# Optimization experiments

Measured on AMD Instinct MI355X. Metric: run time of the kernel, lower is better.

The kernel has to match this reference:

```python
import jax, jax.numpy as jnp
import numpy as np

NEG = -1e30  # finite stand-in for -inf (grad-safe)
GAMMA = 2.0
ALPHA = 1.0


def setup_inputs() -> dict:
    key = jax.random.key(0)
    k1, k2, k3 = jax.random.split(key, 3)
    N, T, C, S = 128, 64, 6625, 25
    logits = jax.random.normal(k1, (N, T, C), dtype=jnp.float32)
    # labels exclude blank (=0)
    targets = jax.random.randint(k2, (N, S), 1, C)
    target_length = jax.random.randint(k3, (N,), 1, S + 1)
    return {"logits": logits, "targets": targets, "target_length": target_length}


def _ctc_nll(log_probs, targets, lengths):
    """log_probs: [N,T,C] (already log-softmaxed). Returns per-sample NLL [N]."""
    N, T, C = log_probs.shape
    S = targets.shape[1]
    S_ext = 2 * S + 1
    # extended label sequence: blank, l1, blank, l2, ..., blank  -> [N, S_ext]
    ext = jnp.zeros((N, S_ext), dtype=targets.dtype).at[:, 1::2].set(targets)
    # gather extended-label log-probs -> [T, N, S_ext]
    idx = jnp.broadcast_to(ext[:, None, :], (N, T, S_ext))
    lp_ext = jnp.transpose(jnp.take_along_axis(log_probs, idx, axis=2), (1, 0, 2))
    # skip transition s-2 -> s allowed iff ext[s] != blank and ext[s] != ext[s-2]
    ext_m2 = jnp.pad(ext[:, :-2], ((0, 0), (2, 0)), constant_values=-1)
    can_skip = (ext != 0) & (ext != ext_m2)  # [N, S_ext]

    alpha0 = (jnp.full((N, S_ext), NEG, dtype=log_probs.dtype)
              .at[:, 0].set(lp_ext[0, :, 0])
              .at[:, 1].set(lp_ext[0, :, 1]))

    def step(alpha, lp_t):
        a1 = alpha
        a2 = jnp.pad(alpha[:, :-1], ((0, 0), (1, 0)), constant_values=NEG)
        a3 = jnp.where(can_skip,
                       jnp.pad(alpha[:, :-2], ((0, 0), (2, 0)), constant_values=NEG),
                       NEG)
        new = jnp.logaddexp(jnp.logaddexp(a1, a2), a3) + lp_t
        return new, None

    alphaT, _ = jax.lax.scan(step, alpha0, lp_ext[1:])
    L = jnp.clip(lengths, 1, T)  # module clamps target_length to [1, T]
    rows = jnp.arange(N)
    ll = jnp.logaddexp(alphaT[rows, 2 * L - 1], alphaT[rows, 2 * L])
    return -ll


def reference(logits, targets, target_length):
    x = jax.nn.log_softmax(logits, axis=2)           # [N,T,C]
    loss = _ctc_nll(x, targets, target_length)        # [N]
    weight = (1.0 - jnp.exp(-loss)) ** GAMMA          # focal reweighting
    loss = loss * weight * ALPHA
    return jnp.mean(loss)
```

## Files before the change

kernel.cpp:

```cpp
#include <hip/hip_runtime.h>
#include <hip/hip_bf16.h>
#include <stdint.h>

#define NN 128
#define TT 64
#define CC 6625
#define SS 25
#define SE 51
#define LPW 26
#define NEGV (-1e30f)

__global__ __launch_bounds__(256) void lse_gather_kernel(
    const float* __restrict__ logits,
    const int*   __restrict__ targets,
    float*       __restrict__ lp)
{
    const int row = blockIdx.x;
    const int tid = threadIdx.x;
    const float* __restrict__ x = logits + (size_t)row * CC;

    const int mis  = (int)(((uintptr_t)x) & 15u) >> 2;
    const int head = (4 - mis) & 3;
    const int nvec = (CC - head) >> 2;
    const int tail = head + (nvec << 2);

    const float4* __restrict__ xv = reinterpret_cast<const float4*>(x + head);

    float4 v[7];
#pragma unroll
    for (int k = 0; k < 7; ++k) {
        const int i = tid + (k << 8);
        if (i < nvec) v[k] = xv[i];
        else          v[k] = make_float4(NEGV, NEGV, NEGV, NEGV);
    }
    const float e0 = (tid < head)       ? x[tid]        : NEGV;
    const float e1 = (tail + tid < CC)  ? x[tail + tid] : NEGV;

    float m = fmaxf(e0, e1);
#pragma unroll
    for (int k = 0; k < 7; ++k) {
        m = fmaxf(m, fmaxf(fmaxf(v[k].x, v[k].y), fmaxf(v[k].z, v[k].w)));
    }
#pragma unroll
    for (int off = 1; off < 64; off <<= 1)
        m = fmaxf(m, __shfl_xor(m, off, 64));

    __shared__ float sm[4];
    __shared__ float ssv[4];
    const int wid = tid >> 6;
    if ((tid & 63) == 0) sm[wid] = m;
    __syncthreads();
    const float M = fmaxf(fmaxf(sm[0], sm[1]), fmaxf(sm[2], sm[3]));

    float s = __expf(e0 - M) + __expf(e1 - M);
#pragma unroll
    for (int k = 0; k < 7; ++k) {
        s += __expf(v[k].x - M) + __expf(v[k].y - M) +
             __expf(v[k].z - M) + __expf(v[k].w - M);
    }
#pragma unroll
    for (int off = 1; off < 64; off <<= 1)
        s += __shfl_xor(s, off, 64);
    if ((tid & 63) == 0) ssv[wid] = s;
    __syncthreads();
    const float S   = ssv[0] + ssv[1] + ssv[2] + ssv[3];
    const float lse = M + __logf(S);

    if (tid < LPW) {
        const int n   = row / TT;
        const int cls = (tid == 0) ? 0 : targets[n * SS + tid - 1];
        lp[(size_t)row * LPW + tid] = x[cls] - lse;
    }
}

__global__ __launch_bounds__(64) void ctc_alpha_kernel(
    const float* __restrict__ lp,
    const int*   __restrict__ targets,
    const int*   __restrict__ target_length,
    float*       __restrict__ out)
{
    const int n = blockIdx.x;
    const int s = threadIdx.x;
    const bool active = (s < SE);

    const int pos = (s & 1) ? (1 + (s >> 1)) : 0;

    bool can_skip = false;
    if (active && (s & 1)) {
        if (s == 1) can_skip = true;
        else {
            const int lab  = targets[n * SS + (s >> 1)];
            const int lab2 = targets[n * SS + (s >> 1) - 1];
            can_skip = (lab != lab2);
        }
    }

    const float* __restrict__ lpn = lp + (size_t)n * TT * LPW;

    float lpt[TT];
#pragma unroll
    for (int t = 0; t < TT; ++t)
        lpt[t] = active ? lpn[t * LPW + pos] : NEGV;

    float alpha = (s < 2) ? lpt[0] : NEGV;

#pragma unroll
    for (int t = 1; t < TT; ++t) {
        const float a1 = alpha;
        float a2 = __shfl_up(alpha, 1, 64);
        if (s == 0) a2 = NEGV;
        float a3 = __shfl_up(alpha, 2, 64);
        if (s < 2 || !can_skip) a3 = NEGV;
        const float mx  = fmaxf(a1, fmaxf(a2, a3));
        const float sum = __expf(a1 - mx) + __expf(a2 - mx) + __expf(a3 - mx);
        alpha = active ? (mx + __logf(sum) + lpt[t]) : NEGV;
    }

    int L = target_length[n];
    L = (L < 1) ? 1 : ((L > SS) ? SS : L);
    const float aL1 = __shfl(alpha, 2 * L - 1, 64);
    const float aL2 = __shfl(alpha, 2 * L,     64);
    if (s == 0) {
        const float mx = fmaxf(aL1, aL2);
        const float ll = mx + __logf(__expf(aL1 - mx) + __expf(aL2 - mx));
        const float loss = -ll;
        const float w = 1.f - __expf(-loss);
        atomicAdd(out, loss * w * w * (1.0f / NN));
    }
}

extern "C" void kernel_launch(void* const* d_in, const int* in_sizes, int n_in,
                              void* d_out, int out_size, void* d_ws, size_t ws_size,
                              hipStream_t stream)
{
    const float* logits  = (const float*)d_in[0];
    const int*   targets = (const int*)  d_in[1];
    const int*   tlen    = (const int*)  d_in[2];
    float*       out     = (float*)d_out;

    float* lp = (float*)d_ws;

    hipMemsetAsync(out, 0, sizeof(float) * out_size, stream);
    lse_gather_kernel<<<NN * TT, 256, 0, stream>>>(logits, targets, lp);
    ctc_alpha_kernel<<<NN, 64, 0, stream>>>(lp, targets, tlen, out);
}
```

Baseline: 307.8 us.

## Fold output zeroing into LSE kernel, transpose lp layout, nontemporal logits loads

The hipMemsetAsync is replaced by zeroing the output inside block 0 of the first kernel, which removes one launch. The gathered label logits are now read before the streaming loop. The logits stream uses nontemporal loads. The lp scratch is stored as [N][LPW][T], so the alpha kernel can read each thread's 64 timesteps with float4 vector loads instead of strided scalar loads. The main cost is about 217 MB of logits read from HBM, so the gains mostly come from lower launch overhead and a cheaper second kernel.

```diff
diff --git a/kernel.cpp b/kernel.cpp
--- a/kernel.cpp
+++ b/kernel.cpp
@@ -10,28 +10,44 @@
 #define LPW 26
 #define NEGV (-1e30f)
 
+typedef float vf4 __attribute__((ext_vector_type(4)));
+
 __global__ __launch_bounds__(256) void lse_gather_kernel(
     const float* __restrict__ logits,
     const int*   __restrict__ targets,
-    float*       __restrict__ lp)
+    float*       __restrict__ lp,
+    float*       __restrict__ out,
+    int          out_elems)
 {
     const int row = blockIdx.x;
     const int tid = threadIdx.x;
     const float* __restrict__ x = logits + (size_t)row * CC;
+
+    if (row == 0) {
+        for (int i = tid; i < out_elems; i += 256) out[i] = 0.f;
+    }
 
     const int mis  = (int)(((uintptr_t)x) & 15u) >> 2;
     const int head = (4 - mis) & 3;
     const int nvec = (CC - head) >> 2;
     const int tail = head + (nvec << 2);
 
-    const float4* __restrict__ xv = reinterpret_cast<const float4*>(x + head);
+    const vf4* __restrict__ xv = reinterpret_cast<const vf4*>(x + head);
 
-    float4 v[7];
+    const int n = row >> 6;
+    const int t = row & 63;
+    float g = 0.f;
+    if (tid < LPW) {
+        const int cls = (tid == 0) ? 0 : targets[n * SS + tid - 1];
+        g = x[cls];
+    }
+
+    vf4 v[7];
 #pragma unroll
     for (int k = 0; k < 7; ++k) {
         const int i = tid + (k << 8);
-        if (i < nvec) v[k] = xv[i];
-        else          v[k] = make_float4(NEGV, NEGV, NEGV, NEGV);
+        if (i < nvec) v[k] = __builtin_nontemporal_load(&xv[i]);
+        else          v[k] = (vf4){NEGV, NEGV, NEGV, NEGV};
     }
     const float e0 = (tid < head)       ? x[tid]        : NEGV;
     const float e1 = (tail + tid < CC)  ? x[tail + tid] : NEGV;
@@ -67,9 +83,7 @@
     const float lse = M + __logf(S);
 
     if (tid < LPW) {
-        const int n   = row / TT;
-        const int cls = (tid == 0) ? 0 : targets[n * SS + tid - 1];
-        lp[(size_t)row * LPW + tid] = x[cls] - lse;
+        lp[((size_t)(n * LPW + tid)) * TT + t] = g - lse;
     }
 }
 
@@ -95,12 +109,22 @@
         }
     }
 
-    const float* __restrict__ lpn = lp + (size_t)n * TT * LPW;
-
     float lpt[TT];
+    if (active) {
+        const vf4* __restrict__ pv =
+            reinterpret_cast<const vf4*>(lp + ((size_t)(n * LPW + pos)) * TT);
 #pragma unroll
-    for (int t = 0; t < TT; ++t)
-        lpt[t] = active ? lpn[t * LPW + pos] : NEGV;
+        for (int k = 0; k < 16; ++k) {
+            const vf4 v4 = pv[k];
+            lpt[4 * k + 0] = v4.x;
+            lpt[4 * k + 1] = v4.y;
+            lpt[4 * k + 2] = v4.z;
+            lpt[4 * k + 3] = v4.w;
+        }
+    } else {
+#pragma unroll
+        for (int t = 0; t < TT; ++t) lpt[t] = NEGV;
+    }
 
     float alpha = (s < 2) ? lpt[0] : NEGV;
 
@@ -140,7 +164,6 @@
 
     float* lp = (float*)d_ws;
 
-    hipMemsetAsync(out, 0, sizeof(float) * out_size, stream);
-    lse_gather_kernel<<<NN * TT, 256, 0, stream>>>(logits, targets, lp);
+    lse_gather_kernel<<<NN * TT, 256, 0, stream>>>(logits, targets, lp, out, out_size);
     ctc_alpha_kernel<<<NN, 64, 0, stream>>>(lp, targets, tlen, out);
 }
```

New measurement: 299.2 us. 1.03x faster.
